# Performance work log

Hardware: AMD Instinct MI355X
Metric: run time of the kernel (lower is better)

The kernel has to match this reference:

```python
import jax, jax.numpy as jnp
import numpy as np

USER_SIZE = 100000
EMBED_DIM = 512
BATCH, SEQ = 16, 2048
N_NODES = BATCH * SEQ          # 32768, adj is [N_NODES, N_NODES]
NNZ = N_NODES * 32             # avg degree 32
LN_EPS = 1e-5


def setup_inputs() -> dict:
    key = jax.random.key(0)
    ks = jax.random.split(key, 6)
    user_ids = jax.random.randint(ks[0], (BATCH, SEQ), 0, USER_SIZE, dtype=jnp.int32)
    adj_row = jax.random.randint(ks[1], (NNZ,), 0, N_NODES, dtype=jnp.int32)
    adj_col = jax.random.randint(ks[2], (NNZ,), 0, N_NODES, dtype=jnp.int32)
    # normalized-adjacency-like positive values, scaled ~1/degree to keep outputs stable
    adj_vals = jax.random.uniform(ks[3], (NNZ,), dtype=jnp.float32) / 32.0
    embedding = jax.random.normal(ks[4], (USER_SIZE, EMBED_DIM), dtype=jnp.float32) * 0.02
    W = jax.random.normal(ks[5], (EMBED_DIM, EMBED_DIM), dtype=jnp.float32) * 0.05
    bias = jnp.zeros((EMBED_DIM,), dtype=jnp.float32)
    ln_gamma = jnp.ones((EMBED_DIM,), dtype=jnp.float32)
    ln_beta = jnp.zeros((EMBED_DIM,), dtype=jnp.float32)
    return {"user_ids": user_ids, "adj_row": adj_row, "adj_col": adj_col,
            "adj_vals": adj_vals, "embedding": embedding, "W": W, "bias": bias,
            "ln_gamma": ln_gamma, "ln_beta": ln_beta}


def reference(user_ids, adj_row, adj_col, adj_vals, embedding, W, bias, ln_gamma, ln_beta):
    # Embedding lookup: [B, S, D]
    x = embedding[user_ids]
    # GCN on flattened nodes: support = X @ W, then sparse adj @ support + bias
    flat = x.reshape(N_NODES, EMBED_DIM)
    support = flat @ W                                  # [N, D]
    msgs = adj_vals[:, None] * support[adj_col]          # [nnz, D]
    agg = jax.ops.segment_sum(msgs, adj_row, num_segments=N_NODES)  # sparse.mm
    out = (agg + bias).reshape(BATCH, SEQ, EMBED_DIM)
    # LayerNorm over last dim
    mu = jnp.mean(out, axis=-1, keepdims=True)
    var = jnp.var(out, axis=-1, keepdims=True)
    out = (out - mu) * jax.lax.rsqrt(var + LN_EPS) * ln_gamma + ln_beta
    # Dropout is identity in eval mode
    return out
```

## Files before the change

### kernel.cpp

```cpp
#include <hip/hip_runtime.h>

#define N_NODES 32768
#define EMBED   512
#define NNZ_TOT 1048576
#define LN_EPS  1e-5f

typedef __attribute__((ext_vector_type(8))) short bf16x8;
typedef __attribute__((ext_vector_type(4))) float f32x4;
typedef __attribute__((ext_vector_type(4))) unsigned int u32x4;

__device__ __forceinline__ unsigned short f2bf(float x) {
    unsigned int u = __float_as_uint(x);
    unsigned int r = u + 0x7fffu + ((u >> 16) & 1u);
    return (unsigned short)(r >> 16);
}
__device__ __forceinline__ unsigned int pk2(float a, float b) {
    return (unsigned int)f2bf(a) | ((unsigned int)f2bf(b) << 16);
}

__global__ void zero_ints(int* __restrict__ p, int n) {
    int i = blockIdx.x * blockDim.x + threadIdx.x;
    if (i < n) p[i] = 0;
}

__global__ __launch_bounds__(256) void wt_kernel(
    const float* __restrict__ W, unsigned short* __restrict__ Wt)
{
    __shared__ float tile[32][33];
    const int tx = threadIdx.x & 31, ty = threadIdx.x >> 5;
    const int kb = blockIdx.y * 32, nb = blockIdx.x * 32;
#pragma unroll
    for (int i = 0; i < 32; i += 8)
        tile[ty + i][tx] = W[(long)(kb + ty + i) * EMBED + nb + tx];
    __syncthreads();
#pragma unroll
    for (int i = 0; i < 32; i += 8)
        Wt[(long)(nb + ty + i) * EMBED + kb + tx] = f2bf(tile[tx][ty + i]);
}

__global__ __launch_bounds__(256) void gemm_mfma(
    const int* __restrict__ uids, const float* __restrict__ emb,
    const unsigned short* __restrict__ Wt, unsigned short* __restrict__ support)
{
    __shared__ unsigned short As[128][40];
    __shared__ unsigned short Bs[128][40];

    const int t  = threadIdx.x;
    const int m0 = blockIdx.y * 128;
    const int n0 = blockIdx.x * 128;

    const int wave = t >> 6;
    const int lane = t & 63;
    const int wm   = (wave & 1) * 64;
    const int wn   = (wave >> 1) * 64;
    const int l16  = lane & 15;
    const int quad = lane >> 4;

    const int srow  = t >> 1;
    const int shalf = (t & 1) * 16;
    const int uid   = uids[m0 + srow];
    const float* arow = emb + (long)uid * EMBED + shalf;
    const unsigned short* brow = Wt + (long)(n0 + srow) * EMBED + shalf;

    f32x4 acc[4][4] = {};

    for (int k0 = 0; k0 < EMBED; k0 += 32) {
        const float4* ap = (const float4*)(arow + k0);
        float4 v0 = ap[0], v1 = ap[1], v2 = ap[2], v3 = ap[3];
        u32x4 lo, hi;
        lo.x = pk2(v0.x, v0.y); lo.y = pk2(v0.z, v0.w);
        lo.z = pk2(v1.x, v1.y); lo.w = pk2(v1.z, v1.w);
        hi.x = pk2(v2.x, v2.y); hi.y = pk2(v2.z, v2.w);
        hi.z = pk2(v3.x, v3.y); hi.w = pk2(v3.z, v3.w);
        *(u32x4*)&As[srow][shalf]     = lo;
        *(u32x4*)&As[srow][shalf + 8] = hi;
        const u32x4* bp = (const u32x4*)(brow + k0);
        *(u32x4*)&Bs[srow][shalf]     = bp[0];
        *(u32x4*)&Bs[srow][shalf + 8] = bp[1];
        __syncthreads();

        bf16x8 af[4], bfr[4];
#pragma unroll
        for (int i = 0; i < 4; ++i)
            af[i] = *(const bf16x8*)&As[wm + i * 16 + l16][quad * 8];
#pragma unroll
        for (int j = 0; j < 4; ++j)
            bfr[j] = *(const bf16x8*)&Bs[wn + j * 16 + l16][quad * 8];
#pragma unroll
        for (int i = 0; i < 4; ++i)
#pragma unroll
            for (int j = 0; j < 4; ++j)
                acc[i][j] = __builtin_amdgcn_mfma_f32_16x16x32_bf16(af[i], bfr[j], acc[i][j], 0, 0, 0);
        __syncthreads();
    }

#pragma unroll
    for (int i = 0; i < 4; ++i) {
#pragma unroll
        for (int j = 0; j < 4; ++j) {
            const int col = n0 + wn + j * 16 + l16;
#pragma unroll
            for (int r = 0; r < 4; ++r) {
                const int row = m0 + wm + i * 16 + quad * 4 + r;
                support[(long)row * EMBED + col] = f2bf(acc[i][j][r]);
            }
        }
    }
}

__global__ void hist_kernel(const int* __restrict__ adj_row, int* __restrict__ counts) {
    int i = blockIdx.x * blockDim.x + threadIdx.x;
    if (i < NNZ_TOT) atomicAdd(&counts[adj_row[i]], 1);
}

__global__ __launch_bounds__(1024) void scan_kernel(
    const int* __restrict__ counts, int* __restrict__ row_start)
{
    __shared__ int ssum[1024];
    const int t = threadIdx.x;
    const int base = t * 32;
    int loc[32];
    int run = 0;
#pragma unroll
    for (int i = 0; i < 32; ++i) {
        int c = counts[base + i];
        loc[i] = run;
        run += c;
    }
    ssum[t] = run;
    __syncthreads();
    for (int off = 1; off < 1024; off <<= 1) {
        int v = (t >= off) ? ssum[t - off] : 0;
        __syncthreads();
        ssum[t] += v;
        __syncthreads();
    }
    int prefix = (t > 0) ? ssum[t - 1] : 0;
#pragma unroll
    for (int i = 0; i < 32; ++i) row_start[base + i] = prefix + loc[i];
    if (t == 1023) row_start[N_NODES] = ssum[1023];
}

__global__ void scatter_kernel(
    const int* __restrict__ adj_row, const int* __restrict__ adj_col,
    const float* __restrict__ adj_vals, const int* __restrict__ row_start,
    int* __restrict__ cursor, int2* __restrict__ sc)
{
    int i = blockIdx.x * blockDim.x + threadIdx.x;
    if (i < NNZ_TOT) {
        int r = adj_row[i];
        int pos = atomicAdd(&cursor[r], 1);
        sc[row_start[r] + pos] = make_int2(adj_col[i], __float_as_int(adj_vals[i]));
    }
}

__global__ __launch_bounds__(256) void agg_ln_v2(
    const int* __restrict__ row_start, const int2* __restrict__ sc,
    const unsigned short* __restrict__ support,
    const float* __restrict__ bias, const float* __restrict__ gamma,
    const float* __restrict__ beta, float* __restrict__ out)
{
    const int n = blockIdx.x;
    const int t = threadIdx.x;
    const int w = t >> 6;
    const int l = t & 63;
    const int s = row_start[n];
    const int e = row_start[n + 1];

    const unsigned short* supp_l = support + l * 8;

    float acc[8] = {};
    int i = s + w;
    for (; i + 4 < e; i += 8) {
        int2 p0 = sc[i];
        int2 p1 = sc[i + 4];
        u32x4 u0 = *(const u32x4*)(supp_l + p0.x * EMBED);
        u32x4 u1 = *(const u32x4*)(supp_l + p1.x * EMBED);
        float v0 = __int_as_float(p0.y);
        float v1 = __int_as_float(p1.y);
#pragma unroll
        for (int j = 0; j < 4; ++j) {
            unsigned int a = u0[j];
            acc[2 * j]     = fmaf(v0, __uint_as_float(a << 16), acc[2 * j]);
            acc[2 * j + 1] = fmaf(v0, __uint_as_float(a & 0xffff0000u), acc[2 * j + 1]);
        }
#pragma unroll
        for (int j = 0; j < 4; ++j) {
            unsigned int a = u1[j];
            acc[2 * j]     = fmaf(v1, __uint_as_float(a << 16), acc[2 * j]);
            acc[2 * j + 1] = fmaf(v1, __uint_as_float(a & 0xffff0000u), acc[2 * j + 1]);
        }
    }
    if (i < e) {
        int2 p0 = sc[i];
        u32x4 u0 = *(const u32x4*)(supp_l + p0.x * EMBED);
        float v0 = __int_as_float(p0.y);
#pragma unroll
        for (int j = 0; j < 4; ++j) {
            unsigned int a = u0[j];
            acc[2 * j]     = fmaf(v0, __uint_as_float(a << 16), acc[2 * j]);
            acc[2 * j + 1] = fmaf(v0, __uint_as_float(a & 0xffff0000u), acc[2 * j + 1]);
        }
    }

    __shared__ float part[4][EMBED];
    *(f32x4*)&part[w][l * 8]     = *(f32x4*)&acc[0];
    *(f32x4*)&part[w][l * 8 + 4] = *(f32x4*)&acc[4];
    __syncthreads();

    const int d = t * 2;
    float x0 = part[0][d] + part[1][d] + part[2][d] + part[3][d] + bias[d];
    float x1 = part[0][d + 1] + part[1][d + 1] + part[2][d + 1] + part[3][d + 1] + bias[d + 1];

    float s1 = x0 + x1;
    float s2 = x0 * x0 + x1 * x1;
#pragma unroll
    for (int off = 32; off > 0; off >>= 1) {
        s1 += __shfl_down(s1, off, 64);
        s2 += __shfl_down(s2, off, 64);
    }
    __shared__ float ws1[4], ws2[4];
    const int wid = t >> 6, lane = t & 63;
    if (lane == 0) { ws1[wid] = s1; ws2[wid] = s2; }
    __syncthreads();
    if (t == 0) {
        ws1[0] = ws1[0] + ws1[1] + ws1[2] + ws1[3];
        ws2[0] = ws2[0] + ws2[1] + ws2[2] + ws2[3];
    }
    __syncthreads();
    const float mean = ws1[0] * (1.f / 512.f);
    const float var  = ws2[0] * (1.f / 512.f) - mean * mean;
    const float rstd = rsqrtf(var + LN_EPS);

    float2 o;
    o.x = (x0 - mean) * rstd * gamma[d] + beta[d];
    o.y = (x1 - mean) * rstd * gamma[d + 1] + beta[d + 1];
    *(float2*)&out[(long)n * EMBED + d] = o;
}

extern "C" void kernel_launch(void* const* d_in, const int* in_sizes, int n_in,
                              void* d_out, int out_size, void* d_ws, size_t ws_size,
                              hipStream_t stream)
{
    const int*   user_ids = (const int*)  d_in[0];
    const int*   adj_row  = (const int*)  d_in[1];
    const int*   adj_col  = (const int*)  d_in[2];
    const float* adj_vals = (const float*)d_in[3];
    const float* emb      = (const float*)d_in[4];
    const float* W        = (const float*)d_in[5];
    const float* bias     = (const float*)d_in[6];
    const float* gamma    = (const float*)d_in[7];
    const float* beta     = (const float*)d_in[8];
    float* out = (float*)d_out;

    char* ws = (char*)d_ws;
    size_t off = 0;
    unsigned short* support = (unsigned short*)(ws + off); off += (size_t)N_NODES * EMBED * 2;
    unsigned short* Wt      = (unsigned short*)(ws + off); off += (size_t)EMBED * EMBED * 2;
    int2*  sc        = (int2*) (ws + off); off += (size_t)NNZ_TOT * 8;
    int*   row_start = (int*)  (ws + off); off += (size_t)(N_NODES + 4) * 4;
    int*   counts    = (int*)  (ws + off); off += (size_t)N_NODES * 4;
    int*   cursor    = (int*)  (ws + off); off += (size_t)N_NODES * 4;
    (void)off; (void)ws_size; (void)in_sizes; (void)n_in; (void)out_size;

    zero_ints<<<(2 * N_NODES + 255) / 256, 256, 0, stream>>>(counts, 2 * N_NODES);

    wt_kernel<<<dim3(16, 16), 256, 0, stream>>>(W, Wt);

    gemm_mfma<<<dim3(EMBED / 128, N_NODES / 128), 256, 0, stream>>>(user_ids, emb, Wt, support);

    hist_kernel<<<NNZ_TOT / 256, 256, 0, stream>>>(adj_row, counts);
    scan_kernel<<<1, 1024, 0, stream>>>(counts, row_start);
    scatter_kernel<<<NNZ_TOT / 256, 256, 0, stream>>>(adj_row, adj_col, adj_vals,
                                                      row_start, cursor, sc);

    agg_ln_v2<<<N_NODES, 256, 0, stream>>>(row_start, sc, support,
                                           bias, gamma, beta, out);
}
```

Measured before the change: 554.6 us.

## Map one wavefront per node in aggregation+LayerNorm, unroll eight-edge gathers

The aggregation/LayerNorm kernel now assigns one 64-lane wavefront per node, four nodes per block, instead of a 256-thread block splitting one node's edges across four waves. This removes the shared-memory partial-sum reduction and all block barriers, since the row sum and sum of squares come from a wave-level xor shuffle. Edge indices and values are made wave-uniform with readfirstlane, and eight support-row gathers are issued before the FMAs to raise memory-level parallelism. The cost is predicated padding loads and zero-weight FMAs on partial batches, plus load imbalance between waves when node degrees differ.

```diff
diff --git a/kernel.cpp b/kernel.cpp
--- a/kernel.cpp
+++ b/kernel.cpp
@@ -154,15 +154,14 @@
     }
 }
 
-__global__ __launch_bounds__(256) void agg_ln_v2(
+__global__ __launch_bounds__(256) void agg_ln_v3(
     const int* __restrict__ row_start, const int2* __restrict__ sc,
     const unsigned short* __restrict__ support,
     const float* __restrict__ bias, const float* __restrict__ gamma,
     const float* __restrict__ beta, float* __restrict__ out)
 {
-    const int n = blockIdx.x;
     const int t = threadIdx.x;
-    const int w = t >> 6;
+    const int n = __builtin_amdgcn_readfirstlane((blockIdx.x << 2) + (t >> 6));
     const int l = t & 63;
     const int s = row_start[n];
     const int e = row_start[n + 1];
@@ -170,72 +169,68 @@
     const unsigned short* supp_l = support + l * 8;
 
     float acc[8] = {};
-    int i = s + w;
-    for (; i + 4 < e; i += 8) {
-        int2 p0 = sc[i];
-        int2 p1 = sc[i + 4];
-        u32x4 u0 = *(const u32x4*)(supp_l + p0.x * EMBED);
-        u32x4 u1 = *(const u32x4*)(supp_l + p1.x * EMBED);
-        float v0 = __int_as_float(p0.y);
-        float v1 = __int_as_float(p1.y);
-#pragma unroll
-        for (int j = 0; j < 4; ++j) {
-            unsigned int a = u0[j];
-            acc[2 * j]     = fmaf(v0, __uint_as_float(a << 16), acc[2 * j]);
-            acc[2 * j + 1] = fmaf(v0, __uint_as_float(a & 0xffff0000u), acc[2 * j + 1]);
+    for (int i = s; i < e; i += 8) {
+        int   col[8];
+        float val[8];
+#pragma unroll
+        for (int j = 0; j < 8; ++j) {
+            const bool ok = (i + j) < e;
+            int2 p = sc[ok ? (i + j) : s];
+            col[j] = __builtin_amdgcn_readfirstlane(p.x);
+            val[j] = __uint_as_float(
+                (unsigned)__builtin_amdgcn_readfirstlane(ok ? p.y : 0));
         }
-#pragma unroll
-        for (int j = 0; j < 4; ++j) {
-            unsigned int a = u1[j];
-            acc[2 * j]     = fmaf(v1, __uint_as_float(a << 16), acc[2 * j]);
-            acc[2 * j + 1] = fmaf(v1, __uint_as_float(a & 0xffff0000u), acc[2 * j + 1]);
+        u32x4 u[8];
+#pragma unroll
+        for (int j = 0; j < 8; ++j)
+            u[j] = *(const u32x4*)(supp_l + col[j] * EMBED);
+#pragma unroll
+        for (int j = 0; j < 8; ++j) {
+            const float v = val[j];
+#pragma unroll
+            for (int q = 0; q < 4; ++q) {
+                unsigned int a = u[j][q];
+                acc[2 * q]     = fmaf(v, __uint_as_float(a << 16), acc[2 * q]);
+                acc[2 * q + 1] = fmaf(v, __uint_as_float(a & 0xffff0000u), acc[2 * q + 1]);
+            }
         }
     }
-    if (i < e) {
-        int2 p0 = sc[i];
-        u32x4 u0 = *(const u32x4*)(supp_l + p0.x * EMBED);
-        float v0 = __int_as_float(p0.y);
-#pragma unroll
-        for (int j = 0; j < 4; ++j) {
-            unsigned int a = u0[j];
-            acc[2 * j]     = fmaf(v0, __uint_as_float(a << 16), acc[2 * j]);
-            acc[2 * j + 1] = fmaf(v0, __uint_as_float(a & 0xffff0000u), acc[2 * j + 1]);
-        }
-    }
-
-    __shared__ float part[4][EMBED];
-    *(f32x4*)&part[w][l * 8]     = *(f32x4*)&acc[0];
-    *(f32x4*)&part[w][l * 8 + 4] = *(f32x4*)&acc[4];
-    __syncthreads();
-
-    const int d = t * 2;
-    float x0 = part[0][d] + part[1][d] + part[2][d] + part[3][d] + bias[d];
-    float x1 = part[0][d + 1] + part[1][d + 1] + part[2][d + 1] + part[3][d + 1] + bias[d + 1];
-
-    float s1 = x0 + x1;
-    float s2 = x0 * x0 + x1 * x1;
+
+    const int d = l * 8;
+    const float4 b0 = *(const float4*)(bias + d);
+    const float4 b1 = *(const float4*)(bias + d + 4);
+    acc[0] += b0.x; acc[1] += b0.y; acc[2] += b0.z; acc[3] += b0.w;
+    acc[4] += b1.x; acc[5] += b1.y; acc[6] += b1.z; acc[7] += b1.w;
+
+    float s1 = 0.f, s2 = 0.f;
+#pragma unroll
+    for (int j = 0; j < 8; ++j) { s1 += acc[j]; s2 = fmaf(acc[j], acc[j], s2); }
 #pragma unroll
     for (int off = 32; off > 0; off >>= 1) {
-        s1 += __shfl_down(s1, off, 64);
-        s2 += __shfl_down(s2, off, 64);
-    }
-    __shared__ float ws1[4], ws2[4];
-    const int wid = t >> 6, lane = t & 63;
-    if (lane == 0) { ws1[wid] = s1; ws2[wid] = s2; }
-    __syncthreads();
-    if (t == 0) {
-        ws1[0] = ws1[0] + ws1[1] + ws1[2] + ws1[3];
-        ws2[0] = ws2[0] + ws2[1] + ws2[2] + ws2[3];
-    }
-    __syncthreads();
-    const float mean = ws1[0] * (1.f / 512.f);
-    const float var  = ws2[0] * (1.f / 512.f) - mean * mean;
+        s1 += __shfl_xor(s1, off, 64);
+        s2 += __shfl_xor(s2, off, 64);
+    }
+    const float mean = s1 * (1.f / 512.f);
+    const float var  = s2 * (1.f / 512.f) - mean * mean;
     const float rstd = rsqrtf(var + LN_EPS);
 
-    float2 o;
-    o.x = (x0 - mean) * rstd * gamma[d] + beta[d];
-    o.y = (x1 - mean) * rstd * gamma[d + 1] + beta[d + 1];
-    *(float2*)&out[(long)n * EMBED + d] = o;
+    const float4 g0  = *(const float4*)(gamma + d);
+    const float4 g1  = *(const float4*)(gamma + d + 4);
+    const float4 be0 = *(const float4*)(beta + d);
+    const float4 be1 = *(const float4*)(beta + d + 4);
+    float4 o0, o1;
+    o0.x = (acc[0] - mean) * rstd * g0.x + be0.x;
+    o0.y = (acc[1] - mean) * rstd * g0.y + be0.y;
+    o0.z = (acc[2] - mean) * rstd * g0.z + be0.z;
+    o0.w = (acc[3] - mean) * rstd * g0.w + be0.w;
+    o1.x = (acc[4] - mean) * rstd * g1.x + be1.x;
+    o1.y = (acc[5] - mean) * rstd * g1.y + be1.y;
+    o1.z = (acc[6] - mean) * rstd * g1.z + be1.z;
+    o1.w = (acc[7] - mean) * rstd * g1.w + be1.w;
+
+    float* orow = out + (long)n * EMBED + d;
+    *(float4*)orow       = o0;
+    *(float4*)(orow + 4) = o1;
 }
 
 extern "C" void kernel_launch(void* const* d_in, const int* in_sizes, int n_in,
@@ -274,6 +269,6 @@
     scatter_kernel<<<NNZ_TOT / 256, 256, 0, stream>>>(adj_row, adj_col, adj_vals,
                                                       row_start, cursor, sc);
 
-    agg_ln_v2<<<N_NODES, 256, 0, stream>>>(row_start, sc, support,
-                                           bias, gamma, beta, out);
-}
+    agg_ln_v3<<<N_NODES / 4, 256, 0, stream>>>(row_start, sc, support,
+                                               bias, gamma, beta, out);
+}
```

After: 565.0 us. No clear change (+1.9%).
